# Optimization experiments

Hardware: AMD Instinct MI355X
Metric: run time of the kernel (lower is better)

The kernel has to match this reference:

```python
import jax, jax.numpy as jnp
import numpy as np

H = 512

def _lstm_cell(x, h, c, Wih, Whh, bih, bhh):
    # PyTorch LSTMCell: gates ordered i, f, g, o
    g = x @ Wih.T + bih + h @ Whh.T + bhh
    i, f, gg, o = jnp.split(g, 4, axis=-1)
    i = jax.nn.sigmoid(i)
    f = jax.nn.sigmoid(f)
    gg = jnp.tanh(gg)
    o = jax.nn.sigmoid(o)
    c_new = f * c + i * gg
    h_new = o * jnp.tanh(c_new)
    return h_new, c_new


def setup_inputs() -> dict:
    key = jax.random.key(0)
    ks = jax.random.split(key, 12)
    B, T = 16, 6574
    s1 = 1.0 / np.sqrt(H)
    u = lambda k, shape: jax.random.uniform(k, shape, jnp.float32, -s1, s1)
    return {
        "input": jax.random.normal(ks[0], (B, T, 2), jnp.float32),
        "W_ih1": u(ks[1], (4 * H, 2)),
        "W_hh1": u(ks[2], (4 * H, H)),
        "b_ih1": u(ks[3], (4 * H,)),
        "b_hh1": u(ks[4], (4 * H,)),
        "W_ih2": u(ks[5], (4 * H, H)),
        "W_hh2": u(ks[6], (4 * H, H)),
        "b_ih2": u(ks[7], (4 * H,)),
        "b_hh2": u(ks[8], (4 * H,)),
        "W_out": u(ks[9], (1, H)),
        "b_out": u(ks[10], (1,)),
    }


def reference(input, W_ih1, W_hh1, b_ih1, b_hh1, W_ih2, W_hh2, b_ih2, b_hh2, W_out, b_out):
    B = input.shape[0]
    h1 = jnp.zeros((B, H), input.dtype)
    c1 = jnp.zeros((B, H), input.dtype)
    h2 = jnp.zeros((B, H), input.dtype)
    c2 = jnp.zeros((B, H), input.dtype)

    def step(carry, x_t):
        h1, c1, h2, c2 = carry
        h1, c1 = _lstm_cell(x_t, h1, c1, W_ih1, W_hh1, b_ih1, b_hh1)
        h2, c2 = _lstm_cell(h1, h2, c2, W_ih2, W_hh2, b_ih2, b_hh2)
        out_t = h2 @ W_out.T + b_out  # [B, 1]
        return (h1, c1, h2, c2), out_t

    xs = jnp.swapaxes(input, 0, 1)  # [T, B, 2]
    _, outs = jax.lax.scan(step, (h1, c1, h2, c2), xs)
    return jnp.swapaxes(outs, 0, 1)  # [B, T, 1]
```

## Files before the change

kernel.cpp:

```cpp
#include <hip/hip_runtime.h>
#include <math.h>

#define NWG  256
#define NTHR 256
#define AGT __HIP_MEMORY_SCOPE_AGENT

#define O_W2  0
#define O_W1  16384
#define O_U   24576
#define O_WX  33280
#define O_B1  33312
#define O_B2  33328
#define O_WO  33344
#define O_XS  33348
#define O_G1  33364
#define O_G2  33492
#define O_C1  33620
#define O_C2  33652
#define LDS_FLOATS 33684

union U64F2 { unsigned long long u; float f[2]; };

__global__ void ws_init_kernel(unsigned* flags, float* h1g, float* h2g,
                               float* out, const float* bout, int n_out) {
    int i = blockIdx.x * blockDim.x + threadIdx.x;
    int n = gridDim.x * blockDim.x;
    float bo = bout[0];
    for (int j = i; j < 512; j += n) flags[j] = 0u;
    for (int j = i; j < 16384; j += n) { h1g[j] = 0.0f; h2g[j] = 0.0f; }
    for (int j = i; j < n_out; j += n) out[j] = bo;
}

__device__ __forceinline__ float sigm(float x) { return 1.0f / (1.0f + __expf(-x)); }
__device__ __forceinline__ float tanh_fast(float x) { return 2.0f / (1.0f + __expf(-2.0f * x)) - 1.0f; }

__device__ __forceinline__ void gbar(unsigned* flags, int wg, int tid, unsigned ph) {
    __syncthreads();
    asm volatile("s_waitcnt vmcnt(0)" ::: "memory");
    const int half = wg & 1;
    if (tid == 0)
        __hip_atomic_store(&flags[(half << 7) + (wg >> 1)], ph, __ATOMIC_RELAXED, AGT);
    if (tid < 32) {
        const unsigned long long* f64 = (const unsigned long long*)flags + (half << 6);
        bool done;
        do {
            unsigned long long v0 = __hip_atomic_load(&f64[2 * tid],     __ATOMIC_RELAXED, AGT);
            unsigned long long v1 = __hip_atomic_load(&f64[2 * tid + 1], __ATOMIC_RELAXED, AGT);
            done = ((unsigned)v0 >= ph) && ((unsigned)(v0 >> 32) >= ph) &&
                   ((unsigned)v1 >= ph) && ((unsigned)(v1 >> 32) >= ph);
            if (!__all(done)) __builtin_amdgcn_s_sleep(1);
        } while (!__all(done));
    }
    __syncthreads();
}

#define STAGE8(srcb, r0,r1,r2,r3,r4,r5,r6,r7)                            \
    asm volatile(                                                         \
        "global_load_dwordx4 %0, %8, off sc0 sc1\n\t"                     \
        "global_load_dwordx4 %1, %9, off sc0 sc1\n\t"                     \
        "global_load_dwordx4 %2, %10, off sc0 sc1\n\t"                    \
        "global_load_dwordx4 %3, %11, off sc0 sc1\n\t"                    \
        "global_load_dwordx4 %4, %12, off sc0 sc1\n\t"                    \
        "global_load_dwordx4 %5, %13, off sc0 sc1\n\t"                    \
        "global_load_dwordx4 %6, %14, off sc0 sc1\n\t"                    \
        "global_load_dwordx4 %7, %15, off sc0 sc1\n\t"                    \
        "s_waitcnt vmcnt(0)"                                              \
        : "=&v"(r0), "=&v"(r1), "=&v"(r2), "=&v"(r3),                     \
          "=&v"(r4), "=&v"(r5), "=&v"(r6), "=&v"(r7)                      \
        : "v"(srcb),        "v"(srcb + 512),  "v"(srcb + 1024),           \
          "v"(srcb + 1536), "v"(srcb + 2048), "v"(srcb + 2560),           \
          "v"(srcb + 3072), "v"(srcb + 3584)                              \
        : "memory")

__global__ __launch_bounds__(NTHR, 1) void lstm_kernel(
    const float* __restrict__ xin,  const float* __restrict__ Wih1,
    const float* __restrict__ Whh1, const float* __restrict__ bih1,
    const float* __restrict__ bhh1, const float* __restrict__ Wih2,
    const float* __restrict__ Whh2, const float* __restrict__ bih2,
    const float* __restrict__ bhh2, const float* __restrict__ Wout,
    const float* __restrict__ bout, float* __restrict__ out,
    unsigned* __restrict__ flags, float* __restrict__ h1g,
    float* __restrict__ h2g, float* __restrict__ outred, int T)
{
    __shared__ float lds[LDS_FLOATS];
    const int tid = threadIdx.x;
    const int wg  = blockIdx.x;
    const int bh  = wg & 1;
    const int jg  = wg >> 1;
    const int j0  = jg * 4;
    const int bd  = bh * 8 + (jg & 7);
    const int jh  = jg >> 3;
    unsigned* flagsA = flags + 256;

    for (int idx = tid; idx < 2048; idx += NTHR) {
        int r = idx >> 7, c4 = idx & 127;
        int grow = (r >> 2) * 512 + j0 + (r & 3);
        *(float4*)&lds[O_W1 + r * 512 + c4 * 4] = *(const float4*)&Whh1[grow * 512 + c4 * 4];
    }
    for (int idx = tid; idx < 4096; idx += NTHR) {
        int r = idx >> 8, c4 = idx & 255;
        int grow = (r >> 2) * 512 + j0 + (r & 3);
        int k = c4 * 4;
        const float* src = (k < 512) ? &Wih2[grow * 512 + k] : &Whh2[grow * 512 + (k - 512)];
        *(float4*)&lds[O_W2 + r * 1024 + k] = *(const float4*)src;
    }
    if (tid < 32) {
        int r = tid >> 1, grow = (r >> 2) * 512 + j0 + (r & 3);
        lds[O_WX + tid] = Wih1[grow * 2 + (tid & 1)];
    }
    if (tid < 16) {
        int grow = (tid >> 2) * 512 + j0 + (tid & 3);
        lds[O_B1 + tid] = bih1[grow] + bhh1[grow];
        lds[O_B2 + tid] = bih2[grow] + bhh2[grow];
    }
    if (tid < 4) lds[O_WO + tid] = Wout[j0 + tid];
    if (tid < 32) { lds[O_C1 + tid] = 0.0f; lds[O_C2 + tid] = 0.0f; }

    if (tid >= 128) {
        const float* srcb = h1g + 1 * 8192 + (bh * 8) * 512 + (tid - 128) * 4;
        float4 r0, r1, r2, r3, r4, r5, r6, r7;
        STAGE8(srcb, r0, r1, r2, r3, r4, r5, r6, r7);
        const int d = (tid - 128) * 4;
        *(float4*)&lds[O_U + 0 * 1024 + d] = r0;
        *(float4*)&lds[O_U + 1 * 1024 + d] = r1;
        *(float4*)&lds[O_U + 2 * 1024 + d] = r2;
        *(float4*)&lds[O_U + 3 * 1024 + d] = r3;
        *(float4*)&lds[O_U + 4 * 1024 + d] = r4;
        *(float4*)&lds[O_U + 5 * 1024 + d] = r5;
        *(float4*)&lds[O_U + 6 * 1024 + d] = r6;
        *(float4*)&lds[O_U + 7 * 1024 + d] = r7;
    }
    __syncthreads();

    const int wv = tid >> 6;
    const int ks = tid & 63;
    unsigned ph = 0;

    float xreg = 0.0f;
    if (tid < 16 && T > 0) {
        int b = tid >> 1, cm = tid & 1;
        xreg = xin[((bh * 8 + b) * (long)T + 0) * 2 + cm];
    }

    for (int s = 0; s <= T; ++s) {
        const int p = s & 1, pq = p ^ 1;

        if (s >= 2 && tid == 0) {
            const unsigned long long* row64 =
                (const unsigned long long*)(outred + pq * 2048 + bd * 128 + jh * 8);
            U64F2 v0; v0.u = __hip_atomic_load(&row64[0], __ATOMIC_RELAXED, AGT);
            U64F2 v1; v1.u = __hip_atomic_load(&row64[1], __ATOMIC_RELAXED, AGT);
            U64F2 v2; v2.u = __hip_atomic_load(&row64[2], __ATOMIC_RELAXED, AGT);
            U64F2 v3; v3.u = __hip_atomic_load(&row64[3], __ATOMIC_RELAXED, AGT);
            float sum = (v0.f[0] + v0.f[1]) + (v1.f[0] + v1.f[1])
                      + (v2.f[0] + v2.f[1]) + (v3.f[0] + v3.f[1]);
            atomicAdd(&out[bd * T + (s - 2)], sum);
        }

        if (tid < 16) {
            if (s < T) lds[O_XS + tid] = xreg;
            if (s + 1 < T) {
                int b = tid >> 1, cm = tid & 1;
                xreg = xin[((bh * 8 + b) * (long)T + (s + 1)) * 2 + cm];
            }
        }

        if (tid < 128) {
            const float* srcb = h2g + pq * 8192 + (bh * 8) * 512 + tid * 4;
            float4 r0, r1, r2, r3, r4, r5, r6, r7;
            STAGE8(srcb, r0, r1, r2, r3, r4, r5, r6, r7);
            const int d = 512 + tid * 4;
            *(float4*)&lds[O_U + 0 * 1024 + d] = r0;
            *(float4*)&lds[O_U + 1 * 1024 + d] = r1;
            *(float4*)&lds[O_U + 2 * 1024 + d] = r2;
            *(float4*)&lds[O_U + 3 * 1024 + d] = r3;
            *(float4*)&lds[O_U + 4 * 1024 + d] = r4;
            *(float4*)&lds[O_U + 5 * 1024 + d] = r5;
            *(float4*)&lds[O_U + 6 * 1024 + d] = r6;
            *(float4*)&lds[O_U + 7 * 1024 + d] = r7;
        }
        __syncthreads();

        float a1[4][8], a2[4][8];
        #pragma unroll
        for (int r = 0; r < 4; ++r)
            #pragma unroll
            for (int b = 0; b < 8; ++b) { a1[r][b] = 0.0f; a2[r][b] = 0.0f; }
        {
            const float* W2b = &lds[O_W2 + wv * 4096];
            const float* W1b = &lds[O_W1 + wv * 2048];
            #pragma unroll
            for (int c = 0; c < 4; ++c) {
                const int k = ks * 4 + c * 256;
                float4 u0 = *(const float4*)&W2b[k];
                float4 u1 = *(const float4*)&W2b[1024 + k];
                float4 u2 = *(const float4*)&W2b[2048 + k];
                float4 u3 = *(const float4*)&W2b[3072 + k];
                float4 w0, w1, w2, w3;
                if (c < 2) {
                    w0 = *(const float4*)&W1b[k];
                    w1 = *(const float4*)&W1b[512 + k];
                    w2 = *(const float4*)&W1b[1024 + k];
                    w3 = *(const float4*)&W1b[1536 + k];
                }
                #pragma unroll
                for (int b = 0; b < 8; ++b) {
                    float4 h = *(const float4*)&lds[O_U + b * 1024 + k];
                    a2[0][b] = fmaf(u0.x,h.x,fmaf(u0.y,h.y,fmaf(u0.z,h.z,fmaf(u0.w,h.w,a2[0][b]))));
                    a2[1][b] = fmaf(u1.x,h.x,fmaf(u1.y,h.y,fmaf(u1.z,h.z,fmaf(u1.w,h.w,a2[1][b]))));
                    a2[2][b] = fmaf(u2.x,h.x,fmaf(u2.y,h.y,fmaf(u2.z,h.z,fmaf(u2.w,h.w,a2[2][b]))));
                    a2[3][b] = fmaf(u3.x,h.x,fmaf(u3.y,h.y,fmaf(u3.z,h.z,fmaf(u3.w,h.w,a2[3][b]))));
                    if (c < 2) {
                        a1[0][b] = fmaf(w0.x,h.x,fmaf(w0.y,h.y,fmaf(w0.z,h.z,fmaf(w0.w,h.w,a1[0][b]))));
                        a1[1][b] = fmaf(w1.x,h.x,fmaf(w1.y,h.y,fmaf(w1.z,h.z,fmaf(w1.w,h.w,a1[1][b]))));
                        a1[2][b] = fmaf(w2.x,h.x,fmaf(w2.y,h.y,fmaf(w2.z,h.z,fmaf(w2.w,h.w,a1[2][b]))));
                        a1[3][b] = fmaf(w3.x,h.x,fmaf(w3.y,h.y,fmaf(w3.z,h.z,fmaf(w3.w,h.w,a1[3][b]))));
                    }
                }
            }
        }
        __syncthreads();

        #pragma unroll
        for (int r = 0; r < 4; ++r)
            #pragma unroll
            for (int b = 0; b < 8; ++b)
                lds[O_U + ((wv * 4 + r) * 8 + b) * 68 + ks] = a1[r][b];
        __syncthreads();
        {
            int o = tid >> 1, hf = tid & 1;
            const float* rr = &lds[O_U + o * 68 + hf * 32];
            float sum = 0.0f;
            #pragma unroll
            for (int c = 0; c < 8; ++c) { float4 v = *(const float4*)&rr[c * 4]; sum += v.x + v.y + v.z + v.w; }
            sum += __shfl_xor(sum, 1);
            if (hf == 0) {
                int r = o >> 3, b = o & 7;
                float g = sum + lds[O_B1 + r]
                        + lds[O_WX + r * 2]     * lds[O_XS + b * 2]
                        + lds[O_WX + r * 2 + 1] * lds[O_XS + b * 2 + 1];
                lds[O_G1 + o] = (wv == 2) ? tanh_fast(g) : sigm(g);
            }
        }
        __syncthreads();

        if (tid < 32 && s < T) {
            int jj = tid >> 3, b = tid & 7;
            float gi = lds[O_G1 + (0 * 4 + jj) * 8 + b];
            float gf = lds[O_G1 + (1 * 4 + jj) * 8 + b];
            float gg = lds[O_G1 + (2 * 4 + jj) * 8 + b];
            float go = lds[O_G1 + (3 * 4 + jj) * 8 + b];
            float c  = gf * lds[O_C1 + tid] + gi * gg;
            lds[O_C1 + tid] = c;
            __hip_atomic_store(&h1g[p * 8192 + (bh * 8 + b) * 512 + j0 + jj],
                               go * tanh_fast(c), __ATOMIC_RELAXED, AGT);
        }

        #pragma unroll
        for (int r = 0; r < 4; ++r)
            #pragma unroll
            for (int b = 0; b < 8; ++b)
                lds[O_U + ((wv * 4 + r) * 8 + b) * 68 + ks] = a2[r][b];

        if (tid < 64 && s < T) {
            asm volatile("s_waitcnt vmcnt(0)" ::: "memory");
            if (tid == 0)
                __hip_atomic_store(&flagsA[((wg & 1) << 7) + (wg >> 1)],
                                   (unsigned)(s + 1), __ATOMIC_RELAXED, AGT);
        }
        __syncthreads();
        {
            int o = tid >> 1, hf = tid & 1;
            const float* rr = &lds[O_U + o * 68 + hf * 32];
            float sum = 0.0f;
            #pragma unroll
            for (int c = 0; c < 8; ++c) { float4 v = *(const float4*)&rr[c * 4]; sum += v.x + v.y + v.z + v.w; }
            sum += __shfl_xor(sum, 1);
            if (hf == 0) {
                float g = sum + lds[O_B2 + (o >> 3)];
                lds[O_G2 + o] = (wv == 2) ? tanh_fast(g) : sigm(g);
            }
        }
        __syncthreads();

        if (tid >= 32 && tid < 64 && s >= 1) {
            int t2 = tid - 32, jj = t2 >> 3, b = t2 & 7;
            float gi = lds[O_G2 + (0 * 4 + jj) * 8 + b];
            float gf = lds[O_G2 + (1 * 4 + jj) * 8 + b];
            float gg = lds[O_G2 + (2 * 4 + jj) * 8 + b];
            float go = lds[O_G2 + (3 * 4 + jj) * 8 + b];
            float c  = gf * lds[O_C2 + t2] + gi * gg;
            lds[O_C2 + t2] = c;
            float h = go * tanh_fast(c);
            __hip_atomic_store(&h2g[p * 8192 + (bh * 8 + b) * 512 + j0 + jj],
                               h, __ATOMIC_RELAXED, AGT);
            float hn = lds[O_WO + jj] * h;
            hn += __shfl_xor(hn, 8);
            hn += __shfl_xor(hn, 16);
            if (jj == 0)
                __hip_atomic_store(&outred[p * 2048 + (bh * 8 + b) * 128 + jg],
                                   hn, __ATOMIC_RELAXED, AGT);
        }

        if (tid >= 128 && s < T) {
            const unsigned long long* fA64 =
                (const unsigned long long*)flagsA + ((wg & 1) << 6);
            const unsigned tgt = (unsigned)(s + 1);
            int l = tid & 63;
            bool ok;
            do {
                unsigned long long v = __hip_atomic_load(&fA64[l], __ATOMIC_RELAXED, AGT);
                ok = ((unsigned)v >= tgt) && ((unsigned)(v >> 32) >= tgt);
                if (!__all(ok)) __builtin_amdgcn_s_sleep(1);
            } while (!__all(ok));
            const float* srcb = h1g + p * 8192 + (bh * 8) * 512 + (tid - 128) * 4;
            float4 r0, r1, r2, r3, r4, r5, r6, r7;
            STAGE8(srcb, r0, r1, r2, r3, r4, r5, r6, r7);
            const int d = (tid - 128) * 4;
            *(float4*)&lds[O_U + 0 * 1024 + d] = r0;
            *(float4*)&lds[O_U + 1 * 1024 + d] = r1;
            *(float4*)&lds[O_U + 2 * 1024 + d] = r2;
            *(float4*)&lds[O_U + 3 * 1024 + d] = r3;
            *(float4*)&lds[O_U + 4 * 1024 + d] = r4;
            *(float4*)&lds[O_U + 5 * 1024 + d] = r5;
            *(float4*)&lds[O_U + 6 * 1024 + d] = r6;
            *(float4*)&lds[O_U + 7 * 1024 + d] = r7;
        }

        gbar(flags, wg, tid, ++ph);
    }

    if (tid == 0) {
        const unsigned long long* row64 =
            (const unsigned long long*)(outred + (T & 1) * 2048 + bd * 128 + jh * 8);
        U64F2 v0; v0.u = __hip_atomic_load(&row64[0], __ATOMIC_RELAXED, AGT);
        U64F2 v1; v1.u = __hip_atomic_load(&row64[1], __ATOMIC_RELAXED, AGT);
        U64F2 v2; v2.u = __hip_atomic_load(&row64[2], __ATOMIC_RELAXED, AGT);
        U64F2 v3; v3.u = __hip_atomic_load(&row64[3], __ATOMIC_RELAXED, AGT);
        float sum = (v0.f[0] + v0.f[1]) + (v1.f[0] + v1.f[1])
                  + (v2.f[0] + v2.f[1]) + (v3.f[0] + v3.f[1]);
        atomicAdd(&out[bd * T + (T - 1)], sum);
    }
}

extern "C" void kernel_launch(void* const* d_in, const int* in_sizes, int n_in,
                              void* d_out, int out_size, void* d_ws, size_t ws_size,
                              hipStream_t stream) {
    const float* xin  = (const float*)d_in[0];
    const float* Wih1 = (const float*)d_in[1];
    const float* Whh1 = (const float*)d_in[2];
    const float* bih1 = (const float*)d_in[3];
    const float* bhh1 = (const float*)d_in[4];
    const float* Wih2 = (const float*)d_in[5];
    const float* Whh2 = (const float*)d_in[6];
    const float* bih2 = (const float*)d_in[7];
    const float* bhh2 = (const float*)d_in[8];
    const float* Wout = (const float*)d_in[9];
    const float* bout = (const float*)d_in[10];
    float* outp = (float*)d_out;
    int T = in_sizes[0] / 32;

    unsigned* flags = (unsigned*)d_ws;
    float* h1g    = (float*)d_ws + 4096;
    float* h2g    = h1g + 16384;
    float* outredp= h2g + 16384;

    hipLaunchKernelGGL(ws_init_kernel, dim3(64), dim3(256), 0, stream,
                       flags, h1g, h2g, outp, bout, out_size);

    hipLaunchKernelGGL(lstm_kernel, dim3(NWG), dim3(NTHR), 0, stream,
                       xin, Wih1, Whh1, bih1, bhh1, Wih2, Whh2, bih2, bhh2,
                       Wout, bout, outp, flags, h1g, h2g, outredp, T);
}
```

Baseline: 53.54 ms.

## Reorder per-step schedule to compute layer-1 gates before loading h2 state

The h2 staging load is now issued as asynchronous inline-asm global loads and overlapped with the layer-1 matvec, which only needs h1. The layer-1 partial sums are pre-reduced with a cross-half shuffle into a new dedicated LDS region, so the h1 output and its flag are published before the layer-2 matvec runs. This shortens the critical path of the cross-workgroup dependency on h1 and removes one barrier. The cost is more LDS, a split of the fused matvec loop into two passes over h, and inline asm that relies on cache-coherence modifiers.

```diff
diff --git a/kernel.cpp b/kernel.cpp
--- a/kernel.cpp
+++ b/kernel.cpp
@@ -8,16 +8,17 @@
 #define O_W2  0
 #define O_W1  16384
 #define O_U   24576
-#define O_WX  33280
-#define O_B1  33312
-#define O_B2  33328
-#define O_WO  33344
-#define O_XS  33348
-#define O_G1  33364
-#define O_G2  33492
-#define O_C1  33620
-#define O_C2  33652
-#define LDS_FLOATS 33684
+#define O_R1  33280
+#define O_WX  37888
+#define O_B1  37920
+#define O_B2  37936
+#define O_WO  37952
+#define O_XS  37956
+#define O_G1  37972
+#define O_G2  38100
+#define O_C1  38228
+#define O_C2  38260
+#define LDS_FLOATS 38292
 
 union U64F2 { unsigned long long u; float f[2]; };
 
@@ -134,8 +135,13 @@
 
     const int wv = tid >> 6;
     const int ks = tid & 63;
+
+    const int sd0 = ((0 * 256 + tid) >> 7) * 1024 + 512 + ((0 * 256 + tid) & 127) * 4;
+    const int sd1 = ((1 * 256 + tid) >> 7) * 1024 + 512 + ((1 * 256 + tid) & 127) * 4;
+    const int sd2 = ((2 * 256 + tid) >> 7) * 1024 + 512 + ((2 * 256 + tid) & 127) * 4;
+    const int sd3 = ((3 * 256 + tid) >> 7) * 1024 + 512 + ((3 * 256 + tid) & 127) * 4;
+
     unsigned ph = 0;
-
     float xreg = 0.0f;
     if (tid < 16 && T > 0) {
         int b = tid >> 1, cm = tid & 1;
@@ -165,74 +171,66 @@
             }
         }
 
-        if (tid < 128) {
-            const float* srcb = h2g + pq * 8192 + (bh * 8) * 512 + tid * 4;
-            float4 r0, r1, r2, r3, r4, r5, r6, r7;
-            STAGE8(srcb, r0, r1, r2, r3, r4, r5, r6, r7);
-            const int d = 512 + tid * 4;
-            *(float4*)&lds[O_U + 0 * 1024 + d] = r0;
-            *(float4*)&lds[O_U + 1 * 1024 + d] = r1;
-            *(float4*)&lds[O_U + 2 * 1024 + d] = r2;
-            *(float4*)&lds[O_U + 3 * 1024 + d] = r3;
-            *(float4*)&lds[O_U + 4 * 1024 + d] = r4;
-            *(float4*)&lds[O_U + 5 * 1024 + d] = r5;
-            *(float4*)&lds[O_U + 6 * 1024 + d] = r6;
-            *(float4*)&lds[O_U + 7 * 1024 + d] = r7;
-        }
-        __syncthreads();
-
-        float a1[4][8], a2[4][8];
+        float4 s0v, s1v, s2v, s3v;
+        {
+            const float* h2b = h2g + pq * 8192 + (bh * 8) * 512;
+            asm volatile(
+                "global_load_dwordx4 %0, %4, off sc0 sc1\n\t"
+                "global_load_dwordx4 %1, %5, off sc0 sc1\n\t"
+                "global_load_dwordx4 %2, %6, off sc0 sc1\n\t"
+                "global_load_dwordx4 %3, %7, off sc0 sc1"
+                : "=&v"(s0v), "=&v"(s1v), "=&v"(s2v), "=&v"(s3v)
+                : "v"(h2b + (0 * 256 + tid) * 4), "v"(h2b + (1 * 256 + tid) * 4),
+                  "v"(h2b + (2 * 256 + tid) * 4), "v"(h2b + (3 * 256 + tid) * 4)
+                : "memory");
+        }
+
+        float a1[4][8];
         #pragma unroll
         for (int r = 0; r < 4; ++r)
             #pragma unroll
-            for (int b = 0; b < 8; ++b) { a1[r][b] = 0.0f; a2[r][b] = 0.0f; }
-        {
-            const float* W2b = &lds[O_W2 + wv * 4096];
+            for (int b = 0; b < 8; ++b) a1[r][b] = 0.0f;
+        {
             const float* W1b = &lds[O_W1 + wv * 2048];
             #pragma unroll
-            for (int c = 0; c < 4; ++c) {
+            for (int c = 0; c < 2; ++c) {
                 const int k = ks * 4 + c * 256;
-                float4 u0 = *(const float4*)&W2b[k];
-                float4 u1 = *(const float4*)&W2b[1024 + k];
-                float4 u2 = *(const float4*)&W2b[2048 + k];
-                float4 u3 = *(const float4*)&W2b[3072 + k];
-                float4 w0, w1, w2, w3;
-                if (c < 2) {
-                    w0 = *(const float4*)&W1b[k];
-                    w1 = *(const float4*)&W1b[512 + k];
-                    w2 = *(const float4*)&W1b[1024 + k];
-                    w3 = *(const float4*)&W1b[1536 + k];
-                }
+                float4 w0 = *(const float4*)&W1b[k];
+                float4 w1 = *(const float4*)&W1b[512 + k];
+                float4 w2 = *(const float4*)&W1b[1024 + k];
+                float4 w3 = *(const float4*)&W1b[1536 + k];
                 #pragma unroll
                 for (int b = 0; b < 8; ++b) {
                     float4 h = *(const float4*)&lds[O_U + b * 1024 + k];
-                    a2[0][b] = fmaf(u0.x,h.x,fmaf(u0.y,h.y,fmaf(u0.z,h.z,fmaf(u0.w,h.w,a2[0][b]))));
-                    a2[1][b] = fmaf(u1.x,h.x,fmaf(u1.y,h.y,fmaf(u1.z,h.z,fmaf(u1.w,h.w,a2[1][b]))));
-                    a2[2][b] = fmaf(u2.x,h.x,fmaf(u2.y,h.y,fmaf(u2.z,h.z,fmaf(u2.w,h.w,a2[2][b]))));
-                    a2[3][b] = fmaf(u3.x,h.x,fmaf(u3.y,h.y,fmaf(u3.z,h.z,fmaf(u3.w,h.w,a2[3][b]))));
-                    if (c < 2) {
-                        a1[0][b] = fmaf(w0.x,h.x,fmaf(w0.y,h.y,fmaf(w0.z,h.z,fmaf(w0.w,h.w,a1[0][b]))));
-                        a1[1][b] = fmaf(w1.x,h.x,fmaf(w1.y,h.y,fmaf(w1.z,h.z,fmaf(w1.w,h.w,a1[1][b]))));
-                        a1[2][b] = fmaf(w2.x,h.x,fmaf(w2.y,h.y,fmaf(w2.z,h.z,fmaf(w2.w,h.w,a1[2][b]))));
-                        a1[3][b] = fmaf(w3.x,h.x,fmaf(w3.y,h.y,fmaf(w3.z,h.z,fmaf(w3.w,h.w,a1[3][b]))));
-                    }
+                    a1[0][b] = fmaf(w0.x,h.x,fmaf(w0.y,h.y,fmaf(w0.z,h.z,fmaf(w0.w,h.w,a1[0][b]))));
+                    a1[1][b] = fmaf(w1.x,h.x,fmaf(w1.y,h.y,fmaf(w1.z,h.z,fmaf(w1.w,h.w,a1[1][b]))));
+                    a1[2][b] = fmaf(w2.x,h.x,fmaf(w2.y,h.y,fmaf(w2.z,h.z,fmaf(w2.w,h.w,a1[2][b]))));
+                    a1[3][b] = fmaf(w3.x,h.x,fmaf(w3.y,h.y,fmaf(w3.z,h.z,fmaf(w3.w,h.w,a1[3][b]))));
                 }
             }
         }
-        __syncthreads();
-
         #pragma unroll
         for (int r = 0; r < 4; ++r)
             #pragma unroll
-            for (int b = 0; b < 8; ++b)
-                lds[O_U + ((wv * 4 + r) * 8 + b) * 68 + ks] = a1[r][b];
-        __syncthreads();
+            for (int b = 0; b < 8; ++b) {
+                float v = a1[r][b] + __shfl_xor(a1[r][b], 32);
+                if (ks < 32)
+                    lds[O_R1 + ((wv * 4 + r) * 8 + b) * 36 + ks] = v;
+            }
+
+        asm volatile("s_waitcnt vmcnt(0)" ::: "memory");
+        *(float4*)&lds[O_U + sd0] = s0v;
+        *(float4*)&lds[O_U + sd1] = s1v;
+        *(float4*)&lds[O_U + sd2] = s2v;
+        *(float4*)&lds[O_U + sd3] = s3v;
+        __syncthreads();
+
         {
             int o = tid >> 1, hf = tid & 1;
-            const float* rr = &lds[O_U + o * 68 + hf * 32];
+            const float* rr = &lds[O_R1 + o * 36 + hf * 16];
             float sum = 0.0f;
             #pragma unroll
-            for (int c = 0; c < 8; ++c) { float4 v = *(const float4*)&rr[c * 4]; sum += v.x + v.y + v.z + v.w; }
+            for (int c = 0; c < 4; ++c) { float4 v = *(const float4*)&rr[c * 4]; sum += v.x + v.y + v.z + v.w; }
             sum += __shfl_xor(sum, 1);
             if (hf == 0) {
                 int r = o >> 3, b = o & 7;
@@ -255,19 +253,44 @@
             __hip_atomic_store(&h1g[p * 8192 + (bh * 8 + b) * 512 + j0 + jj],
                                go * tanh_fast(c), __ATOMIC_RELAXED, AGT);
         }
-
-        #pragma unroll
-        for (int r = 0; r < 4; ++r)
-            #pragma unroll
-            for (int b = 0; b < 8; ++b)
-                lds[O_U + ((wv * 4 + r) * 8 + b) * 68 + ks] = a2[r][b];
-
         if (tid < 64 && s < T) {
             asm volatile("s_waitcnt vmcnt(0)" ::: "memory");
             if (tid == 0)
                 __hip_atomic_store(&flagsA[((wg & 1) << 7) + (wg >> 1)],
                                    (unsigned)(s + 1), __ATOMIC_RELAXED, AGT);
         }
+
+        float a2[4][8];
+        #pragma unroll
+        for (int r = 0; r < 4; ++r)
+            #pragma unroll
+            for (int b = 0; b < 8; ++b) a2[r][b] = 0.0f;
+        {
+            const float* W2b = &lds[O_W2 + wv * 4096];
+            #pragma unroll
+            for (int c = 0; c < 4; ++c) {
+                const int k = ks * 4 + c * 256;
+                float4 u0 = *(const float4*)&W2b[k];
+                float4 u1 = *(const float4*)&W2b[1024 + k];
+                float4 u2 = *(const float4*)&W2b[2048 + k];
+                float4 u3 = *(const float4*)&W2b[3072 + k];
+                #pragma unroll
+                for (int b = 0; b < 8; ++b) {
+                    float4 h = *(const float4*)&lds[O_U + b * 1024 + k];
+                    a2[0][b] = fmaf(u0.x,h.x,fmaf(u0.y,h.y,fmaf(u0.z,h.z,fmaf(u0.w,h.w,a2[0][b]))));
+                    a2[1][b] = fmaf(u1.x,h.x,fmaf(u1.y,h.y,fmaf(u1.z,h.z,fmaf(u1.w,h.w,a2[1][b]))));
+                    a2[2][b] = fmaf(u2.x,h.x,fmaf(u2.y,h.y,fmaf(u2.z,h.z,fmaf(u2.w,h.w,a2[2][b]))));
+                    a2[3][b] = fmaf(u3.x,h.x,fmaf(u3.y,h.y,fmaf(u3.z,h.z,fmaf(u3.w,h.w,a2[3][b]))));
+                }
+            }
+        }
+        __syncthreads();
+
+        #pragma unroll
+        for (int r = 0; r < 4; ++r)
+            #pragma unroll
+            for (int b = 0; b < 8; ++b)
+                lds[O_U + ((wv * 4 + r) * 8 + b) * 68 + ks] = a2[r][b];
         __syncthreads();
         {
             int o = tid >> 1, hf = tid & 1;
```

New measurement: 66.42 ms. 1.24x slower.
